# Performance work log

Measured on AMD Instinct MI355X. Metric: run time of the kernel, lower is better.

## Reference

```python
import jax, jax.numpy as jnp
import numpy as np

# NaiveBias with bias_base_type='symmetric', has_bos=False, has_eos=False.
# w: (1, H, S) learned vector; expanded to symmetric Toeplitz bias (H, S, S),
# then contracted with v via einsum 'nlhd,nhlj->njhd' (bias pre-transposed in original).

def setup_inputs() -> dict:
    key = jax.random.key(0)
    k1, k2 = jax.random.split(key)
    B, S, H, D = 2, 2048, 16, 64
    v = jax.random.normal(k1, (B, S, H, D), dtype=jnp.float32)
    w = jax.random.normal(k2, (1, H, S), dtype=jnp.float32) * 0.02
    return {"v": v, "w": w}


def reference(v, w):
    B, S, H, D = v.shape  # no bos/eos -> seq_len == S, w_ sliced to [..., :S] (full w)
    # symmetric extension: w_ext[k] for k in [0, 2S-2], w_ext[S-1+r] = w[|r|]
    w_ext = jnp.concatenate([jnp.flip(w[..., 1:], axis=-1), w], axis=-1)  # (1, H, 2S-1)
    # original: bias[h, j, i] = w_ext[h, S-1-i+j]; transpose(0,1,3,2) -> bias_t[h, l, j] = w_ext[h, S-1-l+j]
    r = jnp.arange(S)
    idx = (S - 1) - r[:, None] + r[None, :]  # (S, S) Toeplitz index map
    bias_t = w_ext[0][:, idx]  # (H, S, S)
    # einsum 'nlhd,nhlj->njhd'; bias is identical across batch (repeat in _process is a copy)
    pbv = jnp.einsum('blhd,hlj->bjhd', v, bias_t)
    return pbv
```

## Files before the change

### kernel.cpp

```cpp
#include <hip/hip_runtime.h>
#include <stdint.h>


#define SS 2048
#define HH 16
#define DD 64

typedef uint32_t u32;
typedef uint16_t u16;
typedef __attribute__((ext_vector_type(8))) short bf16x8;
typedef __attribute__((ext_vector_type(4))) float f32x4;

__device__ __forceinline__ u16 f2bf(float x) {
  u32 u = __float_as_uint(x);
  u = u + 0x7fffu + ((u >> 16) & 1u);
  return (u16)(u >> 16);
}
__device__ __forceinline__ float bf2f(u16 h) {
  return __uint_as_float(((u32)h) << 16);
}
__device__ __forceinline__ void bfsplit(float x, u16& hi, u16& lo) {
  hi = f2bf(x);
  lo = f2bf(x - bf2f(hi));
}

__global__ __launch_bounds__(256) void prep_w(const float* __restrict__ w, u32* __restrict__ upk)
{
  const int h = blockIdx.x;
  const int t = blockIdx.y * 256 + threadIdx.x;
  int r = 2047 - t;
  int idx = r < 0 ? -r : r;
  if (idx > 2047) idx = 2047;
  float x = w[h * SS + idx];
  u16 hi, lo; bfsplit(x, hi, lo);
  upk[h * 4096 + t] = (u32)hi | ((u32)lo << 16);
}

__device__ __forceinline__ void load_afrag(const u32* tab, int t0, bf16x8& hi, bf16x8& lo) {
  u32 d0 = tab[t0 + 0], d1 = tab[t0 + 1], d2 = tab[t0 + 2], d3 = tab[t0 + 3];
  u32 d4 = tab[t0 + 4], d5 = tab[t0 + 5], d6 = tab[t0 + 6], d7 = tab[t0 + 7];
  union { u32 u[4]; bf16x8 v; } H, L;
  H.u[0] = __builtin_amdgcn_perm(d1, d0, 0x05040100u);
  H.u[1] = __builtin_amdgcn_perm(d3, d2, 0x05040100u);
  H.u[2] = __builtin_amdgcn_perm(d5, d4, 0x05040100u);
  H.u[3] = __builtin_amdgcn_perm(d7, d6, 0x05040100u);
  L.u[0] = __builtin_amdgcn_perm(d1, d0, 0x07060302u);
  L.u[1] = __builtin_amdgcn_perm(d3, d2, 0x07060302u);
  L.u[2] = __builtin_amdgcn_perm(d5, d4, 0x07060302u);
  L.u[3] = __builtin_amdgcn_perm(d7, d6, 0x07060302u);
  hi = H.v; lo = L.v;
}

__global__ __launch_bounds__(512, 2) void toeplitz_fused(
    const float* __restrict__ v, const u32* __restrict__ upk, float* __restrict__ out)
{
  __shared__ __align__(16) u32 tab[4096];
  __shared__ __align__(16) u16 vt[2][2][2][64][32];
  __shared__ __align__(16) float red[2][64][16];

  const int tid  = threadIdx.x;
  const int lane = tid & 63;
  const int wv   = tid >> 6;
  const int half = wv >> 2;
  const int oct  = wv & 3;
  const int m    = lane & 15;
  const int g    = lane >> 4;

  const int lin = blockIdx.x;
  const int xcd = lin & 7;
  const int sl  = lin >> 3;
  const int bh  = (xcd << 2) | (sl >> 3);
  const int jt  = sl & 7;
  const int b = bh >> 4, h = bh & 15;

  {
    const u32* src = upk + h * 4096;
    *(uint4*)&tab[tid * 4]        = *(const uint4*)&src[tid * 4];
    *(uint4*)&tab[2048 + tid * 4] = *(const uint4*)&src[2048 + tid * 4];
  }

  const int sd = lane;
  const int sslot = oct ^ ((sd >> 2) & 3);
  u16* wb0 = &vt[half][0][0][sd][sslot * 8];
  u16* wb1 = &vt[half][1][0][sd][sslot * 8];
  const float* gsrc = v + (((size_t)b * SS + half * 1024 + oct * 8) * HH + h) * DD + sd;

  const int bro = m * 32 + ((g ^ ((m >> 2) & 3)) << 3);

  const int jb = jt * 256 + oct * 64;
  const int tA = 2047 - jb - m + 8 * g + half * 1024;

  float r[8];
  #pragma unroll
  for (int i = 0; i < 8; ++i) r[i] = gsrc[i * 1024];

  bf16x8 Ahi[4], Alo[4];
  f32x4 acc[4][4];
  #pragma unroll
  for (int i = 0; i < 4; ++i)
    #pragma unroll
    for (int j = 0; j < 4; ++j)
      acc[i][j] = (f32x4)(0.0f);

  for (int s = 0; s < 32; ++s) {
    u32 ph[4], pl[4];
    #pragma unroll
    for (int i = 0; i < 4; ++i) {
      u16 h0, l0, h1, l1;
      bfsplit(r[2 * i], h0, l0);
      bfsplit(r[2 * i + 1], h1, l1);
      ph[i] = (u32)h0 | ((u32)h1 << 16);
      pl[i] = (u32)l0 | ((u32)l1 << 16);
    }
    u16* wb = (s & 1) ? wb1 : wb0;
    *(uint4*)wb          = *(const uint4*)ph;
    *(uint4*)(wb + 2048) = *(const uint4*)pl;
    __syncthreads();

    if (s < 31) {
      const float* gs = gsrc + (size_t)(s + 1) * 32 * 1024;
      #pragma unroll
      for (int i = 0; i < 8; ++i) r[i] = gs[i * 1024];
    }

    if (s == 0) {
      #pragma unroll
      for (int jf = 0; jf < 4; ++jf)
        load_afrag(tab, tA - 16 * jf, Ahi[jf], Alo[jf]);
    } else {
      bf16x8 t0h = Ahi[0], t0l = Alo[0], t1h = Ahi[1], t1l = Alo[1];
      load_afrag(tab, tA + 32 * s,      Ahi[0], Alo[0]);
      load_afrag(tab, tA + 32 * s - 16, Ahi[1], Alo[1]);
      Ahi[2] = t0h; Alo[2] = t0l;
      Ahi[3] = t1h; Alo[3] = t1l;
    }

    const u16* vb = &vt[half][s & 1][0][0][0];
    #pragma unroll
    for (int nf = 0; nf < 4; ++nf) {
      bf16x8 bhf = *(const bf16x8*)(vb + nf * 512 + bro);
      bf16x8 blf = *(const bf16x8*)(vb + 2048 + nf * 512 + bro);
      #pragma unroll
      for (int jf = 0; jf < 4; ++jf) {
        acc[jf][nf] = __builtin_amdgcn_mfma_f32_16x16x32_bf16(Ahi[jf], bhf, acc[jf][nf], 0, 0, 0);
        acc[jf][nf] = __builtin_amdgcn_mfma_f32_16x16x32_bf16(Ahi[jf], blf, acc[jf][nf], 0, 0, 0);
        acc[jf][nf] = __builtin_amdgcn_mfma_f32_16x16x32_bf16(Alo[jf], bhf, acc[jf][nf], 0, 0, 0);
      }
    }
    __syncthreads();
  }

  #pragma unroll
  for (int jf = 0; jf < 4; ++jf) {
    for (int p = 0; p < 2; ++p) {
      if (half == 1 && (oct >> 1) == p) {
        float* dst = &red[oct & 1][lane][0];
        #pragma unroll
        for (int nf = 0; nf < 4; ++nf)
          *(f32x4*)(dst + nf * 4) = acc[jf][nf];
      }
      __syncthreads();
      if (half == 0 && (oct >> 1) == p) {
        const float* sp = &red[oct & 1][lane][0];
        #pragma unroll
        for (int nf = 0; nf < 4; ++nf) {
          f32x4 c = acc[jf][nf] + *(const f32x4*)(sp + nf * 4);
          #pragma unroll
          for (int q = 0; q < 4; ++q) {
            int j = jb + jf * 16 + g * 4 + q;
            int d = nf * 16 + m;
            out[(((size_t)b * SS + j) * HH + h) * DD + d] = c[q];
          }
        }
      }
      __syncthreads();
    }
  }
}

__global__ __launch_bounds__(256) void fallback_k(const float* __restrict__ v,
                                                  const float* __restrict__ w,
                                                  float* __restrict__ out)
{
  __shared__ float wrow[SS];
  const int t = threadIdx.x;
  const int j0 = blockIdx.x * 64;
  const int bh = blockIdx.y;
  const int b = bh >> 4, h = bh & 15;
  for (int i = t; i < SS; i += 256) wrow[i] = w[h * SS + i];
  __syncthreads();
  const int jj = t >> 6, d = t & 63;
  float acc[16];
  #pragma unroll
  for (int r = 0; r < 16; ++r) acc[r] = 0.f;
  for (int l = 0; l < SS; ++l) {
    float vv = v[(((size_t)b * SS + l) * HH + h) * DD + d];
    #pragma unroll
    for (int r = 0; r < 16; ++r) {
      int dj = l - (j0 + jj * 16 + r);
      acc[r] += wrow[dj < 0 ? -dj : dj] * vv;
    }
  }
  #pragma unroll
  for (int r = 0; r < 16; ++r)
    out[(((size_t)b * SS + (j0 + jj * 16 + r)) * HH + h) * DD + d] = acc[r];
}

extern "C" void kernel_launch(void* const* d_in, const int* in_sizes, int n_in,
                              void* d_out, int out_size, void* d_ws, size_t ws_size,
                              hipStream_t stream)
{
  const float* v = (const float*)d_in[0];
  const float* w = (const float*)d_in[1];
  float* out = (float*)d_out;
  const size_t need = (size_t)HH * 4096 * 4;
  if (ws_size >= need) {
    u32* upk = (u32*)d_ws;
    prep_w<<<dim3(16, 16), 256, 0, stream>>>(w, upk);
    toeplitz_fused<<<dim3(256), 512, 0, stream>>>(v, upk, out);
  } else {
    fallback_k<<<dim3(32, 32), 256, 0, stream>>>(v, w, out);
  }
}
```

Measured before the change: 113.4 us.

## Software-pipeline Toeplitz MFMA loop with one barrier per step and cheaper bf16 split

The main loop is unrolled by two with double register buffers (rX/rY), so each step converts and writes the next V tile to LDS while MFMAs run on the current one. This cuts the two barriers per step down to one. The hi part of the bf16 split becomes a plain truncation done with perm, which is cheaper but rounds differently from before; the low residual still carries the remainder, so accuracy should be roughly unchanged. MFMA sections are raised to higher priority with s_setprio, and the cross-half reduction uses a larger LDS buffer so it finishes in one pass per fragment, at the cost of more registers and LDS.

```diff
diff --git a/kernel.cpp b/kernel.cpp
--- a/kernel.cpp
+++ b/kernel.cpp
@@ -22,6 +22,16 @@
 __device__ __forceinline__ void bfsplit(float x, u16& hi, u16& lo) {
   hi = f2bf(x);
   lo = f2bf(x - bf2f(hi));
+}
+
+__device__ __forceinline__ void split2(float x0, float x1, u32& ph, u32& pl) {
+  u32 u0 = __float_as_uint(x0), u1 = __float_as_uint(x1);
+  float h0 = __uint_as_float(u0 & 0xffff0000u);
+  float h1 = __uint_as_float(u1 & 0xffff0000u);
+  ph = __builtin_amdgcn_perm(u1, u0, 0x07060302u);
+  u32 v0 = __float_as_uint(x0 - h0); v0 += 0x7fffu + ((v0 >> 16) & 1u);
+  u32 v1 = __float_as_uint(x1 - h1); v1 += 0x7fffu + ((v1 >> 16) & 1u);
+  pl = __builtin_amdgcn_perm(v1, v0, 0x07060302u);
 }
 
 __global__ __launch_bounds__(256) void prep_w(const float* __restrict__ w, u32* __restrict__ upk)
@@ -51,12 +61,45 @@
   hi = H.v; lo = L.v;
 }
 
+__device__ __forceinline__ void advance_frags(const u32* tab, int tnext, bf16x8 Ahi[4], bf16x8 Alo[4]) {
+  Ahi[2] = Ahi[0]; Alo[2] = Alo[0];
+  Ahi[3] = Ahi[1]; Alo[3] = Alo[1];
+  load_afrag(tab, tnext,      Ahi[0], Alo[0]);
+  load_afrag(tab, tnext - 16, Ahi[1], Alo[1]);
+}
+
+__device__ __forceinline__ void split_write(const float r[8], u16* wb) {
+  u32 ph[4], pl[4];
+  #pragma unroll
+  for (int i = 0; i < 4; ++i) split2(r[2 * i], r[2 * i + 1], ph[i], pl[i]);
+  *(uint4*)wb          = *(const uint4*)ph;
+  *(uint4*)(wb + 2048) = *(const uint4*)pl;
+}
+
+__device__ __forceinline__ void mma_tile(const u16* vb, int bro,
+                                         const bf16x8 Ahi[4], const bf16x8 Alo[4],
+                                         f32x4 acc[4][4]) {
+  __builtin_amdgcn_s_setprio(1);
+  #pragma unroll
+  for (int nf = 0; nf < 4; ++nf) {
+    bf16x8 bhf = *(const bf16x8*)(vb + nf * 512 + bro);
+    bf16x8 blf = *(const bf16x8*)(vb + 2048 + nf * 512 + bro);
+    #pragma unroll
+    for (int jf = 0; jf < 4; ++jf) {
+      acc[jf][nf] = __builtin_amdgcn_mfma_f32_16x16x32_bf16(Ahi[jf], bhf, acc[jf][nf], 0, 0, 0);
+      acc[jf][nf] = __builtin_amdgcn_mfma_f32_16x16x32_bf16(Ahi[jf], blf, acc[jf][nf], 0, 0, 0);
+      acc[jf][nf] = __builtin_amdgcn_mfma_f32_16x16x32_bf16(Alo[jf], bhf, acc[jf][nf], 0, 0, 0);
+    }
+  }
+  __builtin_amdgcn_s_setprio(0);
+}
+
 __global__ __launch_bounds__(512, 2) void toeplitz_fused(
     const float* __restrict__ v, const u32* __restrict__ upk, float* __restrict__ out)
 {
   __shared__ __align__(16) u32 tab[4096];
   __shared__ __align__(16) u16 vt[2][2][2][64][32];
-  __shared__ __align__(16) float red[2][64][16];
+  __shared__ __align__(16) float red4[4][64][16];
 
   const int tid  = threadIdx.x;
   const int lane = tid & 63;
@@ -90,11 +133,13 @@
   const int jb = jt * 256 + oct * 64;
   const int tA = 2047 - jb - m + 8 * g + half * 1024;
 
-  float r[8];
-  #pragma unroll
-  for (int i = 0; i < 8; ++i) r[i] = gsrc[i * 1024];
-
-  bf16x8 Ahi[4], Alo[4];
+  float rX[8], rY[8];
+  #pragma unroll
+  for (int i = 0; i < 8; ++i) rX[i] = gsrc[i * 1024];
+  #pragma unroll
+  for (int i = 0; i < 8; ++i) rY[i] = gsrc[32768 + i * 1024];
+  split_write(rX, wb0);
+
   f32x4 acc[4][4];
   #pragma unroll
   for (int i = 0; i < 4; ++i)
@@ -102,79 +147,57 @@
     for (int j = 0; j < 4; ++j)
       acc[i][j] = (f32x4)(0.0f);
 
-  for (int s = 0; s < 32; ++s) {
-    u32 ph[4], pl[4];
-    #pragma unroll
-    for (int i = 0; i < 4; ++i) {
-      u16 h0, l0, h1, l1;
-      bfsplit(r[2 * i], h0, l0);
-      bfsplit(r[2 * i + 1], h1, l1);
-      ph[i] = (u32)h0 | ((u32)h1 << 16);
-      pl[i] = (u32)l0 | ((u32)l1 << 16);
-    }
-    u16* wb = (s & 1) ? wb1 : wb0;
-    *(uint4*)wb          = *(const uint4*)ph;
-    *(uint4*)(wb + 2048) = *(const uint4*)pl;
-    __syncthreads();
-
-    if (s < 31) {
-      const float* gs = gsrc + (size_t)(s + 1) * 32 * 1024;
-      #pragma unroll
-      for (int i = 0; i < 8; ++i) r[i] = gs[i * 1024];
-    }
-
-    if (s == 0) {
-      #pragma unroll
-      for (int jf = 0; jf < 4; ++jf)
-        load_afrag(tab, tA - 16 * jf, Ahi[jf], Alo[jf]);
-    } else {
-      bf16x8 t0h = Ahi[0], t0l = Alo[0], t1h = Ahi[1], t1l = Alo[1];
-      load_afrag(tab, tA + 32 * s,      Ahi[0], Alo[0]);
-      load_afrag(tab, tA + 32 * s - 16, Ahi[1], Alo[1]);
-      Ahi[2] = t0h; Alo[2] = t0l;
-      Ahi[3] = t1h; Alo[3] = t1l;
-    }
-
-    const u16* vb = &vt[half][s & 1][0][0][0];
-    #pragma unroll
-    for (int nf = 0; nf < 4; ++nf) {
-      bf16x8 bhf = *(const bf16x8*)(vb + nf * 512 + bro);
-      bf16x8 blf = *(const bf16x8*)(vb + 2048 + nf * 512 + bro);
-      #pragma unroll
-      for (int jf = 0; jf < 4; ++jf) {
-        acc[jf][nf] = __builtin_amdgcn_mfma_f32_16x16x32_bf16(Ahi[jf], bhf, acc[jf][nf], 0, 0, 0);
-        acc[jf][nf] = __builtin_amdgcn_mfma_f32_16x16x32_bf16(Ahi[jf], blf, acc[jf][nf], 0, 0, 0);
-        acc[jf][nf] = __builtin_amdgcn_mfma_f32_16x16x32_bf16(Alo[jf], bhf, acc[jf][nf], 0, 0, 0);
-      }
-    }
+  __syncthreads();
+
+  bf16x8 Ahi[4], Alo[4];
+  #pragma unroll
+  for (int jf = 0; jf < 4; ++jf)
+    load_afrag(tab, tA - 16 * jf, Ahi[jf], Alo[jf]);
+
+  for (int su = 0; su < 16; ++su) {
+    const int s0 = 2 * su;
+    if (su < 15) {
+      const float* gs = gsrc + (size_t)(s0 + 2) * 32768;
+      #pragma unroll
+      for (int i = 0; i < 8; ++i) rX[i] = gs[i * 1024];
+    }
+    split_write(rY, wb1);
+    mma_tile(&vt[half][0][0][0][0], bro, Ahi, Alo, acc);
+    advance_frags(tab, tA + 32 * (s0 + 1), Ahi, Alo);
+    __syncthreads();
+
+    if (su < 15) {
+      const float* gs = gsrc + (size_t)(s0 + 3) * 32768;
+      #pragma unroll
+      for (int i = 0; i < 8; ++i) rY[i] = gs[i * 1024];
+      split_write(rX, wb0);
+    }
+    mma_tile(&vt[half][1][0][0][0], bro, Ahi, Alo, acc);
+    if (su < 15) advance_frags(tab, tA + 32 * (s0 + 2), Ahi, Alo);
     __syncthreads();
   }
 
   #pragma unroll
   for (int jf = 0; jf < 4; ++jf) {
-    for (int p = 0; p < 2; ++p) {
-      if (half == 1 && (oct >> 1) == p) {
-        float* dst = &red[oct & 1][lane][0];
+    if (half == 1) {
+      #pragma unroll
+      for (int nf = 0; nf < 4; ++nf)
+        *(f32x4*)&red4[oct][lane][nf * 4] = acc[jf][nf];
+    }
+    __syncthreads();
+    if (half == 0) {
+      #pragma unroll
+      for (int nf = 0; nf < 4; ++nf) {
+        f32x4 c = acc[jf][nf] + *(const f32x4*)&red4[oct][lane][nf * 4];
         #pragma unroll
-        for (int nf = 0; nf < 4; ++nf)
-          *(f32x4*)(dst + nf * 4) = acc[jf][nf];
-      }
-      __syncthreads();
-      if (half == 0 && (oct >> 1) == p) {
-        const float* sp = &red[oct & 1][lane][0];
-        #pragma unroll
-        for (int nf = 0; nf < 4; ++nf) {
-          f32x4 c = acc[jf][nf] + *(const f32x4*)(sp + nf * 4);
-          #pragma unroll
-          for (int q = 0; q < 4; ++q) {
-            int j = jb + jf * 16 + g * 4 + q;
-            int d = nf * 16 + m;
-            out[(((size_t)b * SS + j) * HH + h) * DD + d] = c[q];
-          }
+        for (int q = 0; q < 4; ++q) {
+          int j = jb + jf * 16 + g * 4 + q;
+          int d = nf * 16 + m;
+          out[(((size_t)b * SS + j) * HH + h) * DD + d] = c[q];
         }
       }
-      __syncthreads();
-    }
+    }
+    __syncthreads();
   }
 }
 
```

Result: no change. 115.3 us (+1.7%).

## Drop v low-part split, retile waves to 128-row j tiles with 4-way l-split

Applied to the files above, without the earlier changes.

Converts v to a single rounded bf16 instead of a hi/lo pair, cutting the MFMAs per fragment from three to two (w stays split). Waves are reorganized so each covers 128 output rows over a quarter of the l range, with 8 A fragments held in registers, 16 steps instead of 32, and a 4-way LDS reduction at the end. This lowers MFMA count and shared-memory traffic, but v now carries only bf16 precision, which may loosen accuracy, and the larger register footprint can hurt occupancy.

```diff
diff --git a/kernel.cpp b/kernel.cpp
--- a/kernel.cpp
+++ b/kernel.cpp
@@ -51,20 +51,31 @@
   hi = H.v; lo = L.v;
 }
 
+__device__ __forceinline__ void pack_write(const float* f, u16* wb) {
+  u32 pk[4];
+  #pragma unroll
+  for (int i = 0; i < 4; ++i) {
+    u32 a = __float_as_uint(f[2 * i]);     a += 0x7fffu + ((a >> 16) & 1u);
+    u32 c = __float_as_uint(f[2 * i + 1]); c += 0x7fffu + ((c >> 16) & 1u);
+    pk[i] = __builtin_amdgcn_perm(c, a, 0x07060302u);
+  }
+  *(uint4*)wb = *(const uint4*)pk;
+}
+
 __global__ __launch_bounds__(512, 2) void toeplitz_fused(
     const float* __restrict__ v, const u32* __restrict__ upk, float* __restrict__ out)
 {
   __shared__ __align__(16) u32 tab[4096];
-  __shared__ __align__(16) u16 vt[2][2][2][64][32];
-  __shared__ __align__(16) float red[2][64][16];
+  __shared__ __align__(16) u16 vt[4][64][32];
+  __shared__ __align__(16) float red[3][2][4][64][4];
 
   const int tid  = threadIdx.x;
   const int lane = tid & 63;
   const int wv   = tid >> 6;
-  const int half = wv >> 2;
-  const int oct  = wv & 3;
+  const int p    = wv & 1;
+  const int q    = wv >> 1;
   const int m    = lane & 15;
-  const int g    = lane >> 4;
+  const int g4   = lane >> 4;
 
   const int lin = blockIdx.x;
   const int xcd = lin & 7;
@@ -79,102 +90,105 @@
     *(uint4*)&tab[2048 + tid * 4] = *(const uint4*)&src[2048 + tid * 4];
   }
 
-  const int sd = lane;
-  const int sslot = oct ^ ((sd >> 2) & 3);
-  u16* wb0 = &vt[half][0][0][sd][sslot * 8];
-  u16* wb1 = &vt[half][1][0][sd][sslot * 8];
-  const float* gsrc = v + (((size_t)b * SS + half * 1024 + oct * 8) * HH + h) * DD + sd;
-
-  const int bro = m * 32 + ((g ^ ((m >> 2) & 3)) << 3);
-
-  const int jb = jt * 256 + oct * 64;
-  const int tA = 2047 - jb - m + 8 * g + half * 1024;
-
-  float r[8];
-  #pragma unroll
-  for (int i = 0; i < 8; ++i) r[i] = gsrc[i * 1024];
-
-  bf16x8 Ahi[4], Alo[4];
-  f32x4 acc[4][4];
-  #pragma unroll
-  for (int i = 0; i < 4; ++i)
+  const int sg = lane & 3;
+  const int dd = lane >> 2;
+  const int d0 = p * 32 + dd;
+  u16* wb_r0 = &vt[q][d0][sg * 8];
+  u16* wb_r1 = &vt[q][d0 + 16][sg * 8];
+  const float* gsrc = v + ((size_t)(b * SS + q * 512 + sg * 8)) * (HH * DD) + h * DD + d0;
+
+  const u16* brd = &vt[q][m][g4 * 8];
+
+  const int jb = jt * 256 + p * 128;
+  const int tA = 2047 - jb - m + 8 * g4 + q * 512;
+
+  float rF[16];
+  {
+    #pragma unroll
+    for (int i = 0; i < 8; ++i) rF[i]     = gsrc[i * 1024];
+    #pragma unroll
+    for (int i = 0; i < 8; ++i) rF[8 + i] = gsrc[16 + i * 1024];
+    pack_write(&rF[0], wb_r0);
+    pack_write(&rF[8], wb_r1);
+  }
+
+  f32x4 acc[8][4];
+  #pragma unroll
+  for (int i = 0; i < 8; ++i)
     #pragma unroll
     for (int j = 0; j < 4; ++j)
       acc[i][j] = (f32x4)(0.0f);
 
-  for (int s = 0; s < 32; ++s) {
-    u32 ph[4], pl[4];
-    #pragma unroll
-    for (int i = 0; i < 4; ++i) {
-      u16 h0, l0, h1, l1;
-      bfsplit(r[2 * i], h0, l0);
-      bfsplit(r[2 * i + 1], h1, l1);
-      ph[i] = (u32)h0 | ((u32)h1 << 16);
-      pl[i] = (u32)l0 | ((u32)l1 << 16);
-    }
-    u16* wb = (s & 1) ? wb1 : wb0;
-    *(uint4*)wb          = *(const uint4*)ph;
-    *(uint4*)(wb + 2048) = *(const uint4*)pl;
-    __syncthreads();
-
-    if (s < 31) {
-      const float* gs = gsrc + (size_t)(s + 1) * 32 * 1024;
-      #pragma unroll
-      for (int i = 0; i < 8; ++i) r[i] = gs[i * 1024];
-    }
-
-    if (s == 0) {
-      #pragma unroll
-      for (int jf = 0; jf < 4; ++jf)
-        load_afrag(tab, tA - 16 * jf, Ahi[jf], Alo[jf]);
-    } else {
-      bf16x8 t0h = Ahi[0], t0l = Alo[0], t1h = Ahi[1], t1l = Alo[1];
-      load_afrag(tab, tA + 32 * s,      Ahi[0], Alo[0]);
-      load_afrag(tab, tA + 32 * s - 16, Ahi[1], Alo[1]);
-      Ahi[2] = t0h; Alo[2] = t0l;
-      Ahi[3] = t1h; Alo[3] = t1l;
-    }
-
-    const u16* vb = &vt[half][s & 1][0][0][0];
+  __syncthreads();
+
+  bf16x8 Ahi[8], Alo[8];
+  #pragma unroll
+  for (int jf = 0; jf < 8; ++jf)
+    load_afrag(tab, tA - 16 * jf, Ahi[jf], Alo[jf]);
+
+  for (int s = 0; s < 16; ++s) {
+    if (s < 15) {
+      const float* gs = gsrc + (size_t)(s + 1) * 32768;
+      #pragma unroll
+      for (int i = 0; i < 8; ++i) rF[i]     = gs[i * 1024];
+      #pragma unroll
+      for (int i = 0; i < 8; ++i) rF[8 + i] = gs[16 + i * 1024];
+    }
+
     #pragma unroll
     for (int nf = 0; nf < 4; ++nf) {
-      bf16x8 bhf = *(const bf16x8*)(vb + nf * 512 + bro);
-      bf16x8 blf = *(const bf16x8*)(vb + 2048 + nf * 512 + bro);
-      #pragma unroll
-      for (int jf = 0; jf < 4; ++jf) {
-        acc[jf][nf] = __builtin_amdgcn_mfma_f32_16x16x32_bf16(Ahi[jf], bhf, acc[jf][nf], 0, 0, 0);
-        acc[jf][nf] = __builtin_amdgcn_mfma_f32_16x16x32_bf16(Ahi[jf], blf, acc[jf][nf], 0, 0, 0);
-        acc[jf][nf] = __builtin_amdgcn_mfma_f32_16x16x32_bf16(Alo[jf], bhf, acc[jf][nf], 0, 0, 0);
+      bf16x8 bb = *(const bf16x8*)(brd + nf * 512);
+      #pragma unroll
+      for (int jf = 0; jf < 8; ++jf) {
+        acc[jf][nf] = __builtin_amdgcn_mfma_f32_16x16x32_bf16(Ahi[jf], bb, acc[jf][nf], 0, 0, 0);
+        acc[jf][nf] = __builtin_amdgcn_mfma_f32_16x16x32_bf16(Alo[jf], bb, acc[jf][nf], 0, 0, 0);
       }
     }
-    __syncthreads();
-  }
-
-  #pragma unroll
-  for (int jf = 0; jf < 4; ++jf) {
-    for (int p = 0; p < 2; ++p) {
-      if (half == 1 && (oct >> 1) == p) {
-        float* dst = &red[oct & 1][lane][0];
+
+    if (s < 15) {
+      Ahi[7] = Ahi[5]; Alo[7] = Alo[5];
+      Ahi[6] = Ahi[4]; Alo[6] = Alo[4];
+      Ahi[5] = Ahi[3]; Alo[5] = Alo[3];
+      Ahi[4] = Ahi[2]; Alo[4] = Alo[2];
+      Ahi[3] = Ahi[1]; Alo[3] = Alo[1];
+      Ahi[2] = Ahi[0]; Alo[2] = Alo[0];
+      const int tn = tA + 32 * (s + 1);
+      load_afrag(tab, tn,      Ahi[0], Alo[0]);
+      load_afrag(tab, tn - 16, Ahi[1], Alo[1]);
+    }
+
+    __syncthreads();
+    if (s < 15) {
+      pack_write(&rF[0], wb_r0);
+      pack_write(&rF[8], wb_r1);
+    }
+    __syncthreads();
+  }
+
+  float* obase = out + ((size_t)b * SS + jb) * (HH * DD) + h * DD + m;
+  #pragma unroll
+  for (int jf = 0; jf < 8; ++jf) {
+    if (q) {
+      #pragma unroll
+      for (int nf = 0; nf < 4; ++nf)
+        *(f32x4*)&red[q - 1][p][nf][lane][0] = acc[jf][nf];
+    }
+    __syncthreads();
+    if (!q) {
+      #pragma unroll
+      for (int nf = 0; nf < 4; ++nf) {
+        f32x4 c = acc[jf][nf];
+        c += *(const f32x4*)&red[0][p][nf][lane][0];
+        c += *(const f32x4*)&red[1][p][nf][lane][0];
+        c += *(const f32x4*)&red[2][p][nf][lane][0];
         #pragma unroll
-        for (int nf = 0; nf < 4; ++nf)
-          *(f32x4*)(dst + nf * 4) = acc[jf][nf];
-      }
-      __syncthreads();
-      if (half == 0 && (oct >> 1) == p) {
-        const float* sp = &red[oct & 1][lane][0];
-        #pragma unroll
-        for (int nf = 0; nf < 4; ++nf) {
-          f32x4 c = acc[jf][nf] + *(const f32x4*)(sp + nf * 4);
-          #pragma unroll
-          for (int q = 0; q < 4; ++q) {
-            int j = jb + jf * 16 + g * 4 + q;
-            int d = nf * 16 + m;
-            out[(((size_t)b * SS + j) * HH + h) * DD + d] = c[q];
-          }
+        for (int qi = 0; qi < 4; ++qi) {
+          int j = jf * 16 + g4 * 4 + qi;
+          obase[(size_t)j * (HH * DD) + nf * 16] = c[qi];
         }
       }
-      __syncthreads();
-    }
+    }
+    __syncthreads();
   }
 }
 
```

Result: faster. 109.2 us (-3.8%).
